# Kernel tuning notes

Measured on AMD Instinct MI355X. Metric: run time of the kernel, lower is better.

Reference implementation:

```python
import jax, jax.numpy as jnp
import numpy as np

N_HEAD = 16  # matches init_kwargs


def _rope_cos_sin(T, head_dim):
    # inv_freq over even indices, as in AdvancedRotaryEmbedding
    inv_freq = 1.0 / (10000.0 ** (jnp.arange(0, head_dim, 2, dtype=jnp.float32) / head_dim))
    t = jnp.arange(T, dtype=jnp.float32)
    freqs = t[:, None] * inv_freq[None, :]  # [T, head_dim/2]
    return jnp.cos(freqs), jnp.sin(freqs)


def _apply_rope(x, cos, sin):
    # x: [B, H, T, D]; cos/sin: [T, D/2] (broadcast over B, H)
    x1, x2 = x[..., 0::2], x[..., 1::2]
    # half-concat layout, faithful to the module's apply_rotary_emb
    return jnp.concatenate([x1 * cos - x2 * sin, x1 * sin + x2 * cos], axis=-1)


def reference(x, Wq, Wk, Wv, Wo):
    B, T, C = x.shape
    H = N_HEAD
    D = C // H
    # QKV projections (torch Linear: y = x @ W.T), then split heads -> [B, H, T, D]
    q = (x @ Wq.T).reshape(B, T, H, D).transpose(0, 2, 1, 3)
    k = (x @ Wk.T).reshape(B, T, H, D).transpose(0, 2, 1, 3)
    v = (x @ Wv.T).reshape(B, T, H, D).transpose(0, 2, 1, 3)
    cos, sin = _rope_cos_sin(T, D)
    cos = cos.astype(x.dtype)
    sin = sin.astype(x.dtype)
    q = _apply_rope(q, cos, sin)
    k = _apply_rope(k, cos, sin)
    # causal SDPA (eval mode -> dropout_p = 0); jax.nn expects [B, T, H, D]
    y = jax.nn.dot_product_attention(
        q.transpose(0, 2, 1, 3),
        k.transpose(0, 2, 1, 3),
        v.transpose(0, 2, 1, 3),
        is_causal=True,
    )  # [B, T, H, D]
    y = y.reshape(B, T, C)
    return y @ Wo.T


def setup_inputs() -> dict:
    key = jax.random.key(0)
    ks = jax.random.split(key, 5)
    B, T, C = 2, 2048, 1024
    s = 1.0 / np.sqrt(C)
    return {
        "x": jax.random.normal(ks[0], (B, T, C), dtype=jnp.float32),
        "Wq": jax.random.normal(ks[1], (C, C), dtype=jnp.float32) * s,
        "Wk": jax.random.normal(ks[2], (C, C), dtype=jnp.float32) * s,
        "Wv": jax.random.normal(ks[3], (C, C), dtype=jnp.float32) * s,
        "Wo": jax.random.normal(ks[4], (C, C), dtype=jnp.float32) * s,
    }
```

## Files before the change

kernel.cpp:

```cpp
#include <hip/hip_runtime.h>
#include <cstdint>
#include <cstddef>

typedef short s16x8 __attribute__((ext_vector_type(8)));
typedef float f32x4 __attribute__((ext_vector_type(4)));

#define MFMA16(a, b, c) __builtin_amdgcn_mfma_f32_16x16x32_bf16((a), (b), (c), 0, 0, 0)

constexpr int LDP = 72;

__device__ __forceinline__ short f2bf(float f) {
    unsigned u = __builtin_bit_cast(unsigned, f);
    u += 0x7FFFu + ((u >> 16) & 1u);
    return (short)(u >> 16);
}
__device__ __forceinline__ float bf2f(short s) {
    unsigned u = ((unsigned)(unsigned short)s) << 16;
    return __builtin_bit_cast(float, u);
}
__device__ __forceinline__ unsigned pack2(float a, float b) {
    return (unsigned)(unsigned short)f2bf(a) | ((unsigned)(unsigned short)f2bf(b) << 16);
}
__device__ __forceinline__ unsigned pack2t(float a, float b) {
    unsigned ua = __builtin_bit_cast(unsigned, a);
    unsigned ub = __builtin_bit_cast(unsigned, b);
    return (ua >> 16) | (ub & 0xFFFF0000u);
}

__device__ __forceinline__ void async_ld16(const void* g, void* l) {
    __builtin_amdgcn_global_load_lds(
        (const __attribute__((address_space(1))) unsigned int*)g,
        (__attribute__((address_space(3))) unsigned int*)l, 16, 0, 0);
}

__global__ __launch_bounds__(256) void convert_kernel(
    const float* __restrict__ x, const float* __restrict__ Wq,
    const float* __restrict__ Wk, const float* __restrict__ Wv,
    const float* __restrict__ Wo, short* __restrict__ xb, short* __restrict__ wb) {
    const size_t f = ((size_t)blockIdx.x * 256 + threadIdx.x) * 8;
    const float* src;
    short* dst;
    if (f < 4194304) { src = x + f; dst = xb + f; }
    else {
        size_t wo = f - 4194304;
        int seg = (int)(wo >> 20);
        const float* ws4[4] = {Wq, Wk, Wv, Wo};
        src = ws4[seg] + (wo & 1048575u);
        dst = wb + wo;
    }
    float4 a = ((const float4*)src)[0];
    float4 b = ((const float4*)src)[1];
    *(uint4*)dst = make_uint4(pack2(a.x, a.y), pack2(a.z, a.w),
                              pack2(b.x, b.y), pack2(b.z, b.w));
}

__global__ __launch_bounds__(256) void qkv_kernel(
    const short* __restrict__ xb, const short* __restrict__ wb,
    short* __restrict__ Qo, short* __restrict__ Ko, short* __restrict__ VTo) {
    __shared__ __align__(16) short sA[128 * 64];
    __shared__ __align__(16) short sB[128 * 64];
    const int tid = threadIdx.x;
    const int w = tid >> 6, lane = tid & 63, quad = lane >> 4, l15 = lane & 15;
    const int wm = w & 1, wn = w >> 1;
    const int bx = blockIdx.x, by = blockIdx.y;
    const int m0 = by * 128;
    const int nb = bx * 128;

    f32x4 acc[4][4];
#pragma unroll
    for (int i = 0; i < 4; i++)
#pragma unroll
        for (int j = 0; j < 4; j++) acc[i][j] = f32x4{0.f, 0.f, 0.f, 0.f};

    for (int kb = 0; kb < 16; kb++) {
        const int k0 = kb * 64;
        if (kb) __syncthreads();
#pragma unroll
        for (int i = 0; i < 4; i++) {
            int c = i * 256 + tid;
            int row = c >> 3, col8 = (c & 7) * 8;
            async_ld16(xb + (size_t)(m0 + row) * 1024 + k0 + col8,
                       &sA[(i * 256 + w * 64) * 8]);
            async_ld16(wb + (size_t)(nb + row) * 1024 + k0 + col8,
                       &sB[(i * 256 + w * 64) * 8]);
        }
        __syncthreads();
#pragma unroll
        for (int ks = 0; ks < 2; ks++) {
            s16x8 av[4], bv[4];
#pragma unroll
            for (int at = 0; at < 4; at++)
                av[at] = *(const s16x8*)&sA[(wm * 64 + at * 16 + l15) * 64 + ks * 32 + quad * 8];
#pragma unroll
            for (int bt = 0; bt < 4; bt++)
                bv[bt] = *(const s16x8*)&sB[(wn * 64 + bt * 16 + l15) * 64 + ks * 32 + quad * 8];
#pragma unroll
            for (int at = 0; at < 4; at++)
#pragma unroll
                for (int bt = 0; bt < 4; bt++)
                    acc[at][bt] = MFMA16(av[at], bv[bt], acc[at][bt]);
        }
    }

    const int wsel = bx >> 3;
    const int h = (bx & 7) * 2 + wn;
    if (wsel == 2) {
#pragma unroll
        for (int at = 0; at < 4; at++) {
            int m = m0 + wm * 64 + at * 16 + quad * 4;
            int b = m >> 11, t0 = m & 2047;
            size_t base = ((size_t)((b * 16 + h) * 64)) * 2048;
#pragma unroll
            for (int bt = 0; bt < 4; bt++) {
                int d = bt * 16 + l15;
                unsigned lo = pack2(acc[at][bt][0], acc[at][bt][1]);
                unsigned hi = pack2(acc[at][bt][2], acc[at][bt][3]);
                *(uint2*)&VTo[base + (size_t)d * 2048 + t0] = make_uint2(lo, hi);
            }
        }
    } else {
        short* Out = (wsel == 0) ? Qo : Ko;
#pragma unroll
        for (int at = 0; at < 4; at++)
#pragma unroll
            for (int r = 0; r < 4; r++) {
                int m = m0 + wm * 64 + at * 16 + quad * 4 + r;
                int b = m >> 11, t = m & 2047;
                size_t base = (((size_t)(b * 16 + h)) * 2048 + t) * 64;
#pragma unroll
                for (int bt = 0; bt < 4; bt++)
                    Out[base + bt * 16 + l15] = f2bf(acc[at][bt][r]);
            }
    }
}

__global__ __launch_bounds__(256) void rope_kernel(short* __restrict__ Q, short* __restrict__ K) {
    const int rid = blockIdx.x * 256 + threadIdx.x;
    const bool isK = (rid & 65536) != 0;
    short* buf = isK ? K : Q;
    const float sc = isK ? 1.0f : 0.18033688011112042f;
    const int r2 = rid & 65535;
    const int t = r2 & 2047;
    short* row = buf + (size_t)r2 * 64;

    unsigned wv[32];
    const uint4* rp = (const uint4*)row;
#pragma unroll
    for (int c = 0; c < 8; c++) {
        uint4 v = rp[c];
        wv[c * 4 + 0] = v.x; wv[c * 4 + 1] = v.y; wv[c * 4 + 2] = v.z; wv[c * 4 + 3] = v.w;
    }
    float y1[32], y2[32];
    const float tf = (float)t;
#pragma unroll
    for (int i = 0; i < 32; i++) {
        float x1 = bf2f((short)(wv[i] & 0xFFFFu));
        float x2 = bf2f((short)(wv[i] >> 16));
        float inv = exp2f((float)i * -0.4152410118609203f);
        float rev = tf * inv * 0.15915494309189535f;
        rev = rev - floorf(rev);
        float sn = __builtin_amdgcn_sinf(rev);
        float cs = __builtin_amdgcn_cosf(rev);
        y1[i] = (x1 * cs - x2 * sn) * sc;
        y2[i] = (x1 * sn + x2 * cs) * sc;
    }
    unsigned ow[32];
#pragma unroll
    for (int i = 0; i < 16; i++) ow[i] = pack2(y1[2 * i], y1[2 * i + 1]);
#pragma unroll
    for (int i = 0; i < 16; i++) ow[16 + i] = pack2(y2[2 * i], y2[2 * i + 1]);
    uint4* wp = (uint4*)row;
#pragma unroll
    for (int c = 0; c < 8; c++)
        wp[c] = make_uint4(ow[c * 4 + 0], ow[c * 4 + 1], ow[c * 4 + 2], ow[c * 4 + 3]);
}

__global__ __launch_bounds__(256) void attn_kernel(
    const short* __restrict__ Q, const short* __restrict__ K,
    const short* __restrict__ VT, short* __restrict__ paO, float* __restrict__ ml) {
    __shared__ __align__(16) short sQP[64 * LDP];
    __shared__ __align__(16) short sK[64 * LDP];
    __shared__ __align__(16) short sVT[64 * LDP];

    const int tid = threadIdx.x;
    const int w = tid >> 6, lane = tid & 63, quad = lane >> 4, l15 = lane & 15;
    const int u = 79 - blockIdx.x;
    const int bh = blockIdx.y;

    int qt, c;
    if (u < 8)       { qt = u; c = 0; }
    else if (u < 24) { int v = u - 8;  qt = 8 + (v >> 1); c = v & 1; }
    else if (u < 48) { int v = u - 24; qt = 16 + v / 3;   c = v - 3 * (qt - 16); }
    else             { int v = u - 48; qt = 24 + (v >> 2); c = v & 3; }
    const int kt0 = c * 8;
    const int kt1 = min(kt0 + 7, qt);

    const short* Qp = Q + (size_t)bh * 2048 * 64;
    const short* Kp = K + (size_t)bh * 2048 * 64;
    const short* Vp = VT + (size_t)bh * 64 * 2048;

    const int ro = tid >> 3, co = (tid & 7) * 8;

    uint4 rK0 = *(const uint4*)(Kp + (size_t)(kt0 * 64 + ro) * 64 + co);
    uint4 rK1 = *(const uint4*)(Kp + (size_t)(kt0 * 64 + ro + 32) * 64 + co);
    uint4 rV0 = *(const uint4*)(Vp + (size_t)ro * 2048 + kt0 * 64 + co);
    uint4 rV1 = *(const uint4*)(Vp + (size_t)(ro + 32) * 2048 + kt0 * 64 + co);

#pragma unroll
    for (int i = 0; i < 2; i++) {
        int p = tid + i * 256;
        int row = p >> 3, c8 = p & 7;
        uint4 v = *(const uint4*)(Qp + (size_t)(qt * 64 + row) * 64 + c8 * 8);
        *(uint4*)&sQP[row * LDP + c8 * 8] = v;
    }
    __syncthreads();
    s16x8 aq[2];
#pragma unroll
    for (int ks = 0; ks < 2; ks++)
        aq[ks] = *(const s16x8*)&sQP[(w * 16 + l15) * LDP + ks * 32 + quad * 8];

    f32x4 o[4];
#pragma unroll
    for (int i = 0; i < 4; i++) o[i] = f32x4{0.f, 0.f, 0.f, 0.f};
    float mrun = -INFINITY;
    float lrun = 0.f;
    const int q_idx = qt * 64 + w * 16 + l15;

    for (int kt = kt0; kt <= kt1; kt++) {
        __syncthreads();
        *(uint4*)&sK[ro * LDP + co] = rK0;
        *(uint4*)&sK[(ro + 32) * LDP + co] = rK1;
        *(uint4*)&sVT[ro * LDP + co] = rV0;
        *(uint4*)&sVT[(ro + 32) * LDP + co] = rV1;
        const int ktn = (kt < kt1) ? kt + 1 : kt;
        rK0 = *(const uint4*)(Kp + (size_t)(ktn * 64 + ro) * 64 + co);
        rK1 = *(const uint4*)(Kp + (size_t)(ktn * 64 + ro + 32) * 64 + co);
        rV0 = *(const uint4*)(Vp + (size_t)ro * 2048 + ktn * 64 + co);
        rV1 = *(const uint4*)(Vp + (size_t)(ro + 32) * 2048 + ktn * 64 + co);
        __syncthreads();

        f32x4 sa[4];
#pragma unroll
        for (int i = 0; i < 4; i++) sa[i] = f32x4{0.f, 0.f, 0.f, 0.f};
#pragma unroll
        for (int ks = 0; ks < 2; ks++) {
#pragma unroll
            for (int ct = 0; ct < 4; ct++) {
                s16x8 kf = *(const s16x8*)&sK[(ct * 16 + l15) * LDP + ks * 32 + quad * 8];
                sa[ct] = MFMA16(kf, aq[ks], sa[ct]);
            }
        }

        float ps[4][4];
#pragma unroll
        for (int ct = 0; ct < 4; ct++)
#pragma unroll
            for (int r = 0; r < 4; r++) ps[ct][r] = sa[ct][r];

        if (kt == qt) {
#pragma unroll
            for (int ct = 0; ct < 4; ct++) {
                int kbase = kt * 64 + ct * 16 + quad * 4;
#pragma unroll
                for (int r = 0; r < 4; r++)
                    if ((kbase + r) > q_idx) ps[ct][r] = -INFINITY;
            }
        }

        float cm[4];
#pragma unroll
        for (int ct = 0; ct < 4; ct++)
            cm[ct] = fmaxf(fmaxf(ps[ct][0], ps[ct][1]), fmaxf(ps[ct][2], ps[ct][3]));
        float mx = fmaxf(fmaxf(cm[0], cm[1]), fmaxf(cm[2], cm[3]));
        mx = fmaxf(mx, __shfl_xor(mx, 16));
        mx = fmaxf(mx, __shfl_xor(mx, 32));
        float mnew = fmaxf(mrun, mx);
        float alpha = exp2f(mrun - mnew);
        mrun = mnew;
        float cs[4];
#pragma unroll
        for (int ct = 0; ct < 4; ct++) {
#pragma unroll
            for (int r = 0; r < 4; r++) ps[ct][r] = exp2f(ps[ct][r] - mnew);
            cs[ct] = (ps[ct][0] + ps[ct][1]) + (ps[ct][2] + ps[ct][3]);
        }
        float psum = (cs[0] + cs[1]) + (cs[2] + cs[3]);
        psum += __shfl_xor(psum, 16);
        psum += __shfl_xor(psum, 32);
        lrun = lrun * alpha + psum;

        float arow[4];
#pragma unroll
        for (int r = 0; r < 4; r++) arow[r] = __shfl(alpha, quad * 4 + r);
#pragma unroll
        for (int ct = 0; ct < 4; ct++)
#pragma unroll
            for (int r = 0; r < 4; r++) o[ct][r] *= arow[r];

#pragma unroll
        for (int ct = 0; ct < 4; ct++) {
            unsigned lo = pack2t(ps[ct][0], ps[ct][1]);
            unsigned hi = pack2t(ps[ct][2], ps[ct][3]);
            *(uint2*)&sQP[(w * 16 + l15) * LDP + ct * 16 + quad * 4] = make_uint2(lo, hi);
        }

#pragma unroll
        for (int ks2 = 0; ks2 < 2; ks2++) {
            s16x8 pa = *(const s16x8*)&sQP[(w * 16 + l15) * LDP + ks2 * 32 + quad * 8];
#pragma unroll
            for (int ct = 0; ct < 4; ct++) {
                s16x8 vb = *(const s16x8*)&sVT[(ct * 16 + l15) * LDP + ks2 * 32 + quad * 8];
                o[ct] = MFMA16(pa, vb, o[ct]);
            }
        }
    }

    const size_t pbase = ((size_t)(bh * 80 + u)) * 4096;
#pragma unroll
    for (int r = 0; r < 4; r++) {
        int row = w * 16 + quad * 4 + r;
#pragma unroll
        for (int ct = 0; ct < 4; ct++)
            paO[pbase + row * 64 + ct * 16 + l15] = f2bf(o[ct][r]);
    }
    if (quad == 0) {
        int mlbase = (bh * 80 + u) * 128;
        ml[mlbase + w * 16 + l15] = mrun;
        ml[mlbase + 64 + w * 16 + l15] = lrun;
    }
}

__global__ __launch_bounds__(256) void combine_kernel(
    const short* __restrict__ paO, const float* __restrict__ ml, short* __restrict__ Y) {
    const int qt = blockIdx.x, bh = blockIdx.y;
    const int b = bh >> 4, h = bh & 15;
    const int nch = (qt >> 3) + 1;
    int base;
    if (qt < 8) base = qt;
    else if (qt < 16) base = 8 + 2 * (qt - 8);
    else if (qt < 24) base = 24 + 3 * (qt - 16);
    else base = 48 + 4 * (qt - 24);

    const int row = threadIdx.x >> 2;
    const int cq = (threadIdx.x & 3) * 16;

    float mi[4], li[4];
    float M = -INFINITY;
    for (int i = 0; i < nch; i++) {
        int mlbase = (bh * 80 + base + i) * 128;
        mi[i] = ml[mlbase + row];
        li[i] = ml[mlbase + 64 + row];
        M = fmaxf(M, mi[i]);
    }
    float L = 0.f, ai[4];
    for (int i = 0; i < nch; i++) {
        ai[i] = exp2f(mi[i] - M);
        L += li[i] * ai[i];
    }
    const float inv = 1.0f / L;

    float acc[16];
#pragma unroll
    for (int j = 0; j < 16; j++) acc[j] = 0.f;
    for (int i = 0; i < nch; i++) {
        const short* p = paO + ((size_t)(bh * 80 + base + i)) * 4096 + row * 64 + cq;
        uint4 v0 = ((const uint4*)p)[0];
        uint4 v1 = ((const uint4*)p)[1];
        unsigned vs[8] = {v0.x, v0.y, v0.z, v0.w, v1.x, v1.y, v1.z, v1.w};
#pragma unroll
        for (int j = 0; j < 8; j++) {
            acc[2 * j + 0] += bf2f((short)(vs[j] & 0xFFFFu)) * ai[i];
            acc[2 * j + 1] += bf2f((short)(vs[j] >> 16)) * ai[i];
        }
    }
    const int t = qt * 64 + row;
    short* yp = Y + ((size_t)(b * 2048 + t)) * 1024 + h * 64 + cq;
    unsigned ow[8];
#pragma unroll
    for (int j = 0; j < 8; j++) ow[j] = pack2(acc[2 * j] * inv, acc[2 * j + 1] * inv);
    ((uint4*)yp)[0] = make_uint4(ow[0], ow[1], ow[2], ow[3]);
    ((uint4*)yp)[1] = make_uint4(ow[4], ow[5], ow[6], ow[7]);
}

__global__ __launch_bounds__(256) void oproj_kernel(
    const short* __restrict__ Yb, const short* __restrict__ Wob, float* __restrict__ out) {
    __shared__ __align__(16) short sA[64 * 64];
    __shared__ __align__(16) short sB[128 * 64];
    const int tid = threadIdx.x;
    const int w = tid >> 6, lane = tid & 63, quad = lane >> 4, l15 = lane & 15;
    const int m0 = blockIdx.y * 64;
    const int nb = blockIdx.x * 128;

    f32x4 acc[4][2];
#pragma unroll
    for (int i = 0; i < 4; i++)
#pragma unroll
        for (int j = 0; j < 2; j++) acc[i][j] = f32x4{0.f, 0.f, 0.f, 0.f};

    for (int kb = 0; kb < 16; kb++) {
        const int k0 = kb * 64;
        if (kb) __syncthreads();
#pragma unroll
        for (int i = 0; i < 2; i++) {
            int c = i * 256 + tid;
            int row = c >> 3, col8 = (c & 7) * 8;
            async_ld16(Yb + (size_t)(m0 + row) * 1024 + k0 + col8,
                       &sA[(i * 256 + w * 64) * 8]);
        }
#pragma unroll
        for (int i = 0; i < 4; i++) {
            int c = i * 256 + tid;
            int row = c >> 3, col8 = (c & 7) * 8;
            async_ld16(Wob + (size_t)(nb + row) * 1024 + k0 + col8,
                       &sB[(i * 256 + w * 64) * 8]);
        }
        __syncthreads();
#pragma unroll
        for (int ks = 0; ks < 2; ks++) {
            s16x8 av[4], bv[2];
#pragma unroll
            for (int at = 0; at < 4; at++)
                av[at] = *(const s16x8*)&sA[(at * 16 + l15) * 64 + ks * 32 + quad * 8];
#pragma unroll
            for (int bt = 0; bt < 2; bt++)
                bv[bt] = *(const s16x8*)&sB[(w * 32 + bt * 16 + l15) * 64 + ks * 32 + quad * 8];
#pragma unroll
            for (int at = 0; at < 4; at++)
#pragma unroll
                for (int bt = 0; bt < 2; bt++)
                    acc[at][bt] = MFMA16(av[at], bv[bt], acc[at][bt]);
        }
    }
#pragma unroll
    for (int at = 0; at < 4; at++)
#pragma unroll
        for (int r = 0; r < 4; r++) {
            int m = m0 + at * 16 + quad * 4 + r;
#pragma unroll
            for (int bt = 0; bt < 2; bt++) {
                int n = nb + w * 32 + bt * 16 + l15;
                out[(size_t)m * 1024 + n] = acc[at][bt][r];
            }
        }
}

extern "C" void kernel_launch(void* const* d_in, const int* in_sizes, int n_in,
                              void* d_out, int out_size, void* d_ws, size_t ws_size,
                              hipStream_t stream) {
    (void)in_sizes; (void)n_in; (void)out_size; (void)ws_size;
    const float* x  = (const float*)d_in[0];
    const float* Wq = (const float*)d_in[1];
    const float* Wk = (const float*)d_in[2];
    const float* Wv = (const float*)d_in[3];
    const float* Wo = (const float*)d_in[4];
    float* out = (float*)d_out;

    const size_t NE = (size_t)2 * 16 * 2048 * 64;
    short* Q   = (short*)d_ws;
    short* K   = Q + NE;
    short* VT  = K + NE;
    short* Y   = VT + NE;
    short* xb  = Y;
    short* wb  = Y + NE;
    short* paO = wb + NE;
    float* ml  = (float*)(paO + (size_t)32 * 80 * 4096);

    convert_kernel<<<4096, 256, 0, stream>>>(x, Wq, Wk, Wv, Wo, xb, wb);
    qkv_kernel<<<dim3(24, 32), 256, 0, stream>>>(xb, wb, Q, K, VT);
    rope_kernel<<<512, 256, 0, stream>>>(Q, K);
    attn_kernel<<<dim3(80, 32), 256, 0, stream>>>(Q, K, VT, paO, ml);
    combine_kernel<<<dim3(32, 32), 256, 0, stream>>>(paO, ml, Y);
    oproj_kernel<<<dim3(8, 64), 256, 0, stream>>>(Y, wb + 3 * 1048576, out);
}
```

Before: 211.7 us.

## Process two query tiles per attention block to reuse K/V loads

Each attention block now handles 128 query rows (two 64-row groups) against each K/V tile, halving K/V global/LDS traffic per query and doubling MFMA work per barrier. The split-K chunk schedule is recomputed for 128-row query tiles, which halves the grid to 1280 blocks, and the combine kernel is reshaped to match. The register prefetch of the next K/V tile is removed, so loads are now synchronous inside the loop. Register pressure rises and there are fewer blocks in flight. The causal mask also covers more wasted work on the diagonal, since both query groups run every key tile up to 2*qt2+1.

Measured after the change: 234.5 us. 10.8% more time.

```diff
diff --git a/kernel.cpp b/kernel.cpp
--- a/kernel.cpp
+++ b/kernel.cpp
@@ -178,178 +178,200 @@
 __global__ __launch_bounds__(256) void attn_kernel(
     const short* __restrict__ Q, const short* __restrict__ K,
     const short* __restrict__ VT, short* __restrict__ paO, float* __restrict__ ml) {
-    __shared__ __align__(16) short sQP[64 * LDP];
+    __shared__ __align__(16) short sQP[128 * LDP];
     __shared__ __align__(16) short sK[64 * LDP];
     __shared__ __align__(16) short sVT[64 * LDP];
 
     const int tid = threadIdx.x;
     const int w = tid >> 6, lane = tid & 63, quad = lane >> 4, l15 = lane & 15;
-    const int u = 79 - blockIdx.x;
+    const int u = 39 - blockIdx.x;
     const int bh = blockIdx.y;
 
-    int qt, c;
-    if (u < 8)       { qt = u; c = 0; }
-    else if (u < 24) { int v = u - 8;  qt = 8 + (v >> 1); c = v & 1; }
-    else if (u < 48) { int v = u - 24; qt = 16 + v / 3;   c = v - 3 * (qt - 16); }
-    else             { int v = u - 48; qt = 24 + (v >> 2); c = v & 3; }
+    int qt2, c;
+    if (u < 4)       { qt2 = u; c = 0; }
+    else if (u < 12) { int v = u - 4;  qt2 = 4 + (v >> 1); c = v & 1; }
+    else if (u < 24) { int v = u - 12; qt2 = 8 + v / 3;    c = v - 3 * (qt2 - 8); }
+    else             { int v = u - 24; qt2 = 12 + (v >> 2); c = v & 3; }
+    const int ktEnd = 2 * qt2 + 1;
     const int kt0 = c * 8;
-    const int kt1 = min(kt0 + 7, qt);
+    const int kt1 = min(kt0 + 7, ktEnd);
 
     const short* Qp = Q + (size_t)bh * 2048 * 64;
     const short* Kp = K + (size_t)bh * 2048 * 64;
     const short* Vp = VT + (size_t)bh * 64 * 2048;
 
-    const int ro = tid >> 3, co = (tid & 7) * 8;
-
-    uint4 rK0 = *(const uint4*)(Kp + (size_t)(kt0 * 64 + ro) * 64 + co);
-    uint4 rK1 = *(const uint4*)(Kp + (size_t)(kt0 * 64 + ro + 32) * 64 + co);
-    uint4 rV0 = *(const uint4*)(Vp + (size_t)ro * 2048 + kt0 * 64 + co);
-    uint4 rV1 = *(const uint4*)(Vp + (size_t)(ro + 32) * 2048 + kt0 * 64 + co);
-
-#pragma unroll
-    for (int i = 0; i < 2; i++) {
+#pragma unroll
+    for (int i = 0; i < 4; i++) {
         int p = tid + i * 256;
         int row = p >> 3, c8 = p & 7;
-        uint4 v = *(const uint4*)(Qp + (size_t)(qt * 64 + row) * 64 + c8 * 8);
+        uint4 v = *(const uint4*)(Qp + (size_t)(qt2 * 128 + row) * 64 + c8 * 8);
         *(uint4*)&sQP[row * LDP + c8 * 8] = v;
     }
     __syncthreads();
-    s16x8 aq[2];
-#pragma unroll
-    for (int ks = 0; ks < 2; ks++)
-        aq[ks] = *(const s16x8*)&sQP[(w * 16 + l15) * LDP + ks * 32 + quad * 8];
-
-    f32x4 o[4];
-#pragma unroll
-    for (int i = 0; i < 4; i++) o[i] = f32x4{0.f, 0.f, 0.f, 0.f};
-    float mrun = -INFINITY;
-    float lrun = 0.f;
-    const int q_idx = qt * 64 + w * 16 + l15;
+    s16x8 aq[2][2];
+#pragma unroll
+    for (int g = 0; g < 2; g++)
+#pragma unroll
+        for (int ks = 0; ks < 2; ks++)
+            aq[g][ks] = *(const s16x8*)&sQP[(g * 64 + w * 16 + l15) * LDP + ks * 32 + quad * 8];
+
+    f32x4 o[2][4];
+#pragma unroll
+    for (int g = 0; g < 2; g++)
+#pragma unroll
+        for (int i = 0; i < 4; i++) o[g][i] = f32x4{0.f, 0.f, 0.f, 0.f};
+    float mrun[2] = {-INFINITY, -INFINITY};
+    float lrun[2] = {0.f, 0.f};
+    const int qidx0 = qt2 * 128 + w * 16 + l15;
+    const int qidx1 = qidx0 + 64;
 
     for (int kt = kt0; kt <= kt1; kt++) {
         __syncthreads();
-        *(uint4*)&sK[ro * LDP + co] = rK0;
-        *(uint4*)&sK[(ro + 32) * LDP + co] = rK1;
-        *(uint4*)&sVT[ro * LDP + co] = rV0;
-        *(uint4*)&sVT[(ro + 32) * LDP + co] = rV1;
-        const int ktn = (kt < kt1) ? kt + 1 : kt;
-        rK0 = *(const uint4*)(Kp + (size_t)(ktn * 64 + ro) * 64 + co);
-        rK1 = *(const uint4*)(Kp + (size_t)(ktn * 64 + ro + 32) * 64 + co);
-        rV0 = *(const uint4*)(Vp + (size_t)ro * 2048 + ktn * 64 + co);
-        rV1 = *(const uint4*)(Vp + (size_t)(ro + 32) * 2048 + ktn * 64 + co);
+#pragma unroll
+        for (int i = 0; i < 2; i++) {
+            int p = tid + i * 256;
+            int row = p >> 3, c8 = p & 7;
+            uint4 kv = *(const uint4*)(Kp + (size_t)(kt * 64 + row) * 64 + c8 * 8);
+            *(uint4*)&sK[row * LDP + c8 * 8] = kv;
+            uint4 vv = *(const uint4*)(Vp + (size_t)row * 2048 + kt * 64 + c8 * 8);
+            *(uint4*)&sVT[row * LDP + c8 * 8] = vv;
+        }
         __syncthreads();
 
-        f32x4 sa[4];
-#pragma unroll
-        for (int i = 0; i < 4; i++) sa[i] = f32x4{0.f, 0.f, 0.f, 0.f};
+        f32x4 sa[2][4];
+#pragma unroll
+        for (int g = 0; g < 2; g++)
+#pragma unroll
+            for (int i = 0; i < 4; i++) sa[g][i] = f32x4{0.f, 0.f, 0.f, 0.f};
 #pragma unroll
         for (int ks = 0; ks < 2; ks++) {
 #pragma unroll
             for (int ct = 0; ct < 4; ct++) {
                 s16x8 kf = *(const s16x8*)&sK[(ct * 16 + l15) * LDP + ks * 32 + quad * 8];
-                sa[ct] = MFMA16(kf, aq[ks], sa[ct]);
-            }
-        }
-
-        float ps[4][4];
-#pragma unroll
-        for (int ct = 0; ct < 4; ct++)
-#pragma unroll
-            for (int r = 0; r < 4; r++) ps[ct][r] = sa[ct][r];
-
-        if (kt == qt) {
+                sa[0][ct] = MFMA16(kf, aq[0][ks], sa[0][ct]);
+                sa[1][ct] = MFMA16(kf, aq[1][ks], sa[1][ct]);
+            }
+        }
+
+        float ps[2][4][4];
+#pragma unroll
+        for (int g = 0; g < 2; g++)
+#pragma unroll
+            for (int ct = 0; ct < 4; ct++)
+#pragma unroll
+                for (int r = 0; r < 4; r++) ps[g][ct][r] = sa[g][ct][r];
+
+        if (kt >= 2 * qt2) {
 #pragma unroll
             for (int ct = 0; ct < 4; ct++) {
                 int kbase = kt * 64 + ct * 16 + quad * 4;
 #pragma unroll
-                for (int r = 0; r < 4; r++)
-                    if ((kbase + r) > q_idx) ps[ct][r] = -INFINITY;
-            }
-        }
-
-        float cm[4];
-#pragma unroll
-        for (int ct = 0; ct < 4; ct++)
-            cm[ct] = fmaxf(fmaxf(ps[ct][0], ps[ct][1]), fmaxf(ps[ct][2], ps[ct][3]));
-        float mx = fmaxf(fmaxf(cm[0], cm[1]), fmaxf(cm[2], cm[3]));
-        mx = fmaxf(mx, __shfl_xor(mx, 16));
-        mx = fmaxf(mx, __shfl_xor(mx, 32));
-        float mnew = fmaxf(mrun, mx);
-        float alpha = exp2f(mrun - mnew);
-        mrun = mnew;
-        float cs[4];
-#pragma unroll
-        for (int ct = 0; ct < 4; ct++) {
-#pragma unroll
-            for (int r = 0; r < 4; r++) ps[ct][r] = exp2f(ps[ct][r] - mnew);
-            cs[ct] = (ps[ct][0] + ps[ct][1]) + (ps[ct][2] + ps[ct][3]);
-        }
-        float psum = (cs[0] + cs[1]) + (cs[2] + cs[3]);
-        psum += __shfl_xor(psum, 16);
-        psum += __shfl_xor(psum, 32);
-        lrun = lrun * alpha + psum;
-
-        float arow[4];
-#pragma unroll
-        for (int r = 0; r < 4; r++) arow[r] = __shfl(alpha, quad * 4 + r);
-#pragma unroll
-        for (int ct = 0; ct < 4; ct++)
-#pragma unroll
-            for (int r = 0; r < 4; r++) o[ct][r] *= arow[r];
-
-#pragma unroll
-        for (int ct = 0; ct < 4; ct++) {
-            unsigned lo = pack2t(ps[ct][0], ps[ct][1]);
-            unsigned hi = pack2t(ps[ct][2], ps[ct][3]);
-            *(uint2*)&sQP[(w * 16 + l15) * LDP + ct * 16 + quad * 4] = make_uint2(lo, hi);
-        }
+                for (int r = 0; r < 4; r++) {
+                    if ((kbase + r) > qidx0) ps[0][ct][r] = -INFINITY;
+                    if ((kbase + r) > qidx1) ps[1][ct][r] = -INFINITY;
+                }
+            }
+        }
+
+        float alpha[2];
+#pragma unroll
+        for (int g = 0; g < 2; g++) {
+            float cm[4];
+#pragma unroll
+            for (int ct = 0; ct < 4; ct++)
+                cm[ct] = fmaxf(fmaxf(ps[g][ct][0], ps[g][ct][1]), fmaxf(ps[g][ct][2], ps[g][ct][3]));
+            float mx = fmaxf(fmaxf(cm[0], cm[1]), fmaxf(cm[2], cm[3]));
+            mx = fmaxf(mx, __shfl_xor(mx, 16));
+            mx = fmaxf(mx, __shfl_xor(mx, 32));
+            float mnew = fmaxf(mrun[g], mx);
+            alpha[g] = exp2f(mrun[g] - mnew);
+            mrun[g] = mnew;
+            float cs[4];
+#pragma unroll
+            for (int ct = 0; ct < 4; ct++) {
+#pragma unroll
+                for (int r = 0; r < 4; r++) ps[g][ct][r] = exp2f(ps[g][ct][r] - mnew);
+                cs[ct] = (ps[g][ct][0] + ps[g][ct][1]) + (ps[g][ct][2] + ps[g][ct][3]);
+            }
+            float psum = (cs[0] + cs[1]) + (cs[2] + cs[3]);
+            psum += __shfl_xor(psum, 16);
+            psum += __shfl_xor(psum, 32);
+            lrun[g] = lrun[g] * alpha[g] + psum;
+        }
+
+#pragma unroll
+        for (int g = 0; g < 2; g++) {
+            float arow[4];
+#pragma unroll
+            for (int r = 0; r < 4; r++) arow[r] = __shfl(alpha[g], quad * 4 + r);
+#pragma unroll
+            for (int ct = 0; ct < 4; ct++)
+#pragma unroll
+                for (int r = 0; r < 4; r++) o[g][ct][r] *= arow[r];
+        }
+
+#pragma unroll
+        for (int g = 0; g < 2; g++)
+#pragma unroll
+            for (int ct = 0; ct < 4; ct++) {
+                unsigned lo = pack2t(ps[g][ct][0], ps[g][ct][1]);
+                unsigned hi = pack2t(ps[g][ct][2], ps[g][ct][3]);
+                *(uint2*)&sQP[(g * 64 + w * 16 + l15) * LDP + ct * 16 + quad * 4] = make_uint2(lo, hi);
+            }
 
 #pragma unroll
         for (int ks2 = 0; ks2 < 2; ks2++) {
-            s16x8 pa = *(const s16x8*)&sQP[(w * 16 + l15) * LDP + ks2 * 32 + quad * 8];
+            s16x8 pa0 = *(const s16x8*)&sQP[(w * 16 + l15) * LDP + ks2 * 32 + quad * 8];
+            s16x8 pa1 = *(const s16x8*)&sQP[(64 + w * 16 + l15) * LDP + ks2 * 32 + quad * 8];
 #pragma unroll
             for (int ct = 0; ct < 4; ct++) {
                 s16x8 vb = *(const s16x8*)&sVT[(ct * 16 + l15) * LDP + ks2 * 32 + quad * 8];
-                o[ct] = MFMA16(pa, vb, o[ct]);
-            }
-        }
-    }
-
-    const size_t pbase = ((size_t)(bh * 80 + u)) * 4096;
-#pragma unroll
-    for (int r = 0; r < 4; r++) {
-        int row = w * 16 + quad * 4 + r;
-#pragma unroll
-        for (int ct = 0; ct < 4; ct++)
-            paO[pbase + row * 64 + ct * 16 + l15] = f2bf(o[ct][r]);
-    }
+                o[0][ct] = MFMA16(pa0, vb, o[0][ct]);
+                o[1][ct] = MFMA16(pa1, vb, o[1][ct]);
+            }
+        }
+    }
+
+    const size_t pbase = ((size_t)(bh * 40 + u)) * 8192;
+#pragma unroll
+    for (int g = 0; g < 2; g++)
+#pragma unroll
+        for (int r = 0; r < 4; r++) {
+            int row = g * 64 + w * 16 + quad * 4 + r;
+#pragma unroll
+            for (int ct = 0; ct < 4; ct++)
+                paO[pbase + row * 64 + ct * 16 + l15] = f2bf(o[g][ct][r]);
+        }
     if (quad == 0) {
-        int mlbase = (bh * 80 + u) * 128;
-        ml[mlbase + w * 16 + l15] = mrun;
-        ml[mlbase + 64 + w * 16 + l15] = lrun;
+        int mlbase = (bh * 40 + u) * 256;
+#pragma unroll
+        for (int g = 0; g < 2; g++) {
+            ml[mlbase + g * 64 + w * 16 + l15] = mrun[g];
+            ml[mlbase + 128 + g * 64 + w * 16 + l15] = lrun[g];
+        }
     }
 }
 
 __global__ __launch_bounds__(256) void combine_kernel(
     const short* __restrict__ paO, const float* __restrict__ ml, short* __restrict__ Y) {
-    const int qt = blockIdx.x, bh = blockIdx.y;
+    const int qt2 = blockIdx.x, bh = blockIdx.y;
     const int b = bh >> 4, h = bh & 15;
-    const int nch = (qt >> 3) + 1;
+    const int nch = (qt2 >> 2) + 1;
     int base;
-    if (qt < 8) base = qt;
-    else if (qt < 16) base = 8 + 2 * (qt - 8);
-    else if (qt < 24) base = 24 + 3 * (qt - 16);
-    else base = 48 + 4 * (qt - 24);
-
-    const int row = threadIdx.x >> 2;
-    const int cq = (threadIdx.x & 3) * 16;
+    if (qt2 < 4) base = qt2;
+    else if (qt2 < 8) base = 4 + 2 * (qt2 - 4);
+    else if (qt2 < 12) base = 12 + 3 * (qt2 - 8);
+    else base = 24 + 4 * (qt2 - 12);
+
+    const int row = threadIdx.x >> 1;
+    const int cq = (threadIdx.x & 1) * 32;
 
     float mi[4], li[4];
     float M = -INFINITY;
     for (int i = 0; i < nch; i++) {
-        int mlbase = (bh * 80 + base + i) * 128;
+        int mlbase = (bh * 40 + base + i) * 256;
         mi[i] = ml[mlbase + row];
-        li[i] = ml[mlbase + 64 + row];
+        li[i] = ml[mlbase + 128 + row];
         M = fmaxf(M, mi[i]);
     }
     float L = 0.f, ai[4];
@@ -359,27 +381,32 @@
     }
     const float inv = 1.0f / L;
 
-    float acc[16];
-#pragma unroll
-    for (int j = 0; j < 16; j++) acc[j] = 0.f;
+    float acc[32];
+#pragma unroll
+    for (int j = 0; j < 32; j++) acc[j] = 0.f;
     for (int i = 0; i < nch; i++) {
-        const short* p = paO + ((size_t)(bh * 80 + base + i)) * 4096 + row * 64 + cq;
-        uint4 v0 = ((const uint4*)p)[0];
-        uint4 v1 = ((const uint4*)p)[1];
-        unsigned vs[8] = {v0.x, v0.y, v0.z, v0.w, v1.x, v1.y, v1.z, v1.w};
-#pragma unroll
-        for (int j = 0; j < 8; j++) {
-            acc[2 * j + 0] += bf2f((short)(vs[j] & 0xFFFFu)) * ai[i];
-            acc[2 * j + 1] += bf2f((short)(vs[j] >> 16)) * ai[i];
-        }
-    }
-    const int t = qt * 64 + row;
+        const short* p = paO + ((size_t)(bh * 40 + base + i)) * 8192 + row * 64 + cq;
+#pragma unroll
+        for (int q = 0; q < 4; q++) {
+            uint4 v = ((const uint4*)p)[q];
+            unsigned vs[4] = {v.x, v.y, v.z, v.w};
+#pragma unroll
+            for (int j = 0; j < 4; j++) {
+                acc[q * 8 + 2 * j + 0] += bf2f((short)(vs[j] & 0xFFFFu)) * ai[i];
+                acc[q * 8 + 2 * j + 1] += bf2f((short)(vs[j] >> 16)) * ai[i];
+            }
+        }
+    }
+    const int t = qt2 * 128 + row;
     short* yp = Y + ((size_t)(b * 2048 + t)) * 1024 + h * 64 + cq;
-    unsigned ow[8];
-#pragma unroll
-    for (int j = 0; j < 8; j++) ow[j] = pack2(acc[2 * j] * inv, acc[2 * j + 1] * inv);
-    ((uint4*)yp)[0] = make_uint4(ow[0], ow[1], ow[2], ow[3]);
-    ((uint4*)yp)[1] = make_uint4(ow[4], ow[5], ow[6], ow[7]);
+#pragma unroll
+    for (int q = 0; q < 4; q++) {
+        unsigned ow[4];
+#pragma unroll
+        for (int j = 0; j < 4; j++)
+            ow[j] = pack2(acc[q * 8 + 2 * j] * inv, acc[q * 8 + 2 * j + 1] * inv);
+        ((uint4*)yp)[q] = make_uint4(ow[0], ow[1], ow[2], ow[3]);
+    }
 }
 
 __global__ __launch_bounds__(256) void oproj_kernel(
@@ -463,12 +490,12 @@
     short* xb  = Y;
     short* wb  = Y + NE;
     short* paO = wb + NE;
-    float* ml  = (float*)(paO + (size_t)32 * 80 * 4096);
+    float* ml  = (float*)(paO + (size_t)32 * 40 * 8192);
 
     convert_kernel<<<4096, 256, 0, stream>>>(x, Wq, Wk, Wv, Wo, xb, wb);
     qkv_kernel<<<dim3(24, 32), 256, 0, stream>>>(xb, wb, Q, K, VT);
     rope_kernel<<<512, 256, 0, stream>>>(Q, K);
-    attn_kernel<<<dim3(80, 32), 256, 0, stream>>>(Q, K, VT, paO, ml);
-    combine_kernel<<<dim3(32, 32), 256, 0, stream>>>(paO, ml, Y);
+    attn_kernel<<<dim3(40, 32), 256, 0, stream>>>(Q, K, VT, paO, ml);
+    combine_kernel<<<dim3(16, 32), 256, 0, stream>>>(paO, ml, Y);
     oproj_kernel<<<dim3(8, 64), 256, 0, stream>>>(Y, wb + 3 * 1048576, out);
 }
```

## Widen attention KV tile to 128 keys and drop register prefetch

Applied to the files above, without the earlier changes.

Each attention loop iteration now processes 128 keys instead of 64, with a wider LDS stride for the P and V^T buffers. The register-staged prefetch of the next K/V tile is replaced by direct global-to-LDS loads inside the loop. This halves the loop iterations and barrier/softmax-reduction overhead per key. In exchange it loses load/compute overlap, raises LDS use and register pressure, and computes masked keys beyond the diagonal.

Result: no change. 212.4 us (+0.3%).

```diff
diff --git a/kernel.cpp b/kernel.cpp
--- a/kernel.cpp
+++ b/kernel.cpp
@@ -8,6 +8,7 @@
 #define MFMA16(a, b, c) __builtin_amdgcn_mfma_f32_16x16x32_bf16((a), (b), (c), 0, 0, 0)
 
 constexpr int LDP = 72;
+constexpr int LDW = 136;
 
 __device__ __forceinline__ short f2bf(float f) {
     unsigned u = __builtin_bit_cast(unsigned, f);
@@ -178,9 +179,9 @@
 __global__ __launch_bounds__(256) void attn_kernel(
     const short* __restrict__ Q, const short* __restrict__ K,
     const short* __restrict__ VT, short* __restrict__ paO, float* __restrict__ ml) {
-    __shared__ __align__(16) short sQP[64 * LDP];
-    __shared__ __align__(16) short sK[64 * LDP];
-    __shared__ __align__(16) short sVT[64 * LDP];
+    __shared__ __align__(16) short sQP[64 * LDW];
+    __shared__ __align__(16) short sK[128 * LDP];
+    __shared__ __align__(16) short sVT[64 * LDW];
 
     const int tid = threadIdx.x;
     const int w = tid >> 6, lane = tid & 63, quad = lane >> 4, l15 = lane & 15;
@@ -192,32 +193,26 @@
     else if (u < 24) { int v = u - 8;  qt = 8 + (v >> 1); c = v & 1; }
     else if (u < 48) { int v = u - 24; qt = 16 + v / 3;   c = v - 3 * (qt - 16); }
     else             { int v = u - 48; qt = 24 + (v >> 2); c = v & 3; }
-    const int kt0 = c * 8;
-    const int kt1 = min(kt0 + 7, qt);
+    const int kbDiag = qt >> 1;
+    const int kb0 = c * 4;
+    const int kb1 = min(kb0 + 3, kbDiag);
 
     const short* Qp = Q + (size_t)bh * 2048 * 64;
     const short* Kp = K + (size_t)bh * 2048 * 64;
     const short* Vp = VT + (size_t)bh * 64 * 2048;
-
-    const int ro = tid >> 3, co = (tid & 7) * 8;
-
-    uint4 rK0 = *(const uint4*)(Kp + (size_t)(kt0 * 64 + ro) * 64 + co);
-    uint4 rK1 = *(const uint4*)(Kp + (size_t)(kt0 * 64 + ro + 32) * 64 + co);
-    uint4 rV0 = *(const uint4*)(Vp + (size_t)ro * 2048 + kt0 * 64 + co);
-    uint4 rV1 = *(const uint4*)(Vp + (size_t)(ro + 32) * 2048 + kt0 * 64 + co);
 
 #pragma unroll
     for (int i = 0; i < 2; i++) {
         int p = tid + i * 256;
         int row = p >> 3, c8 = p & 7;
         uint4 v = *(const uint4*)(Qp + (size_t)(qt * 64 + row) * 64 + c8 * 8);
-        *(uint4*)&sQP[row * LDP + c8 * 8] = v;
+        *(uint4*)&sQP[row * LDW + c8 * 8] = v;
     }
     __syncthreads();
     s16x8 aq[2];
 #pragma unroll
     for (int ks = 0; ks < 2; ks++)
-        aq[ks] = *(const s16x8*)&sQP[(w * 16 + l15) * LDP + ks * 32 + quad * 8];
+        aq[ks] = *(const s16x8*)&sQP[(w * 16 + l15) * LDW + ks * 32 + quad * 8];
 
     f32x4 o[4];
 #pragma unroll
@@ -226,65 +221,70 @@
     float lrun = 0.f;
     const int q_idx = qt * 64 + w * 16 + l15;
 
-    for (int kt = kt0; kt <= kt1; kt++) {
+    for (int kb = kb0; kb <= kb1; kb++) {
         __syncthreads();
-        *(uint4*)&sK[ro * LDP + co] = rK0;
-        *(uint4*)&sK[(ro + 32) * LDP + co] = rK1;
-        *(uint4*)&sVT[ro * LDP + co] = rV0;
-        *(uint4*)&sVT[(ro + 32) * LDP + co] = rV1;
-        const int ktn = (kt < kt1) ? kt + 1 : kt;
-        rK0 = *(const uint4*)(Kp + (size_t)(ktn * 64 + ro) * 64 + co);
-        rK1 = *(const uint4*)(Kp + (size_t)(ktn * 64 + ro + 32) * 64 + co);
-        rV0 = *(const uint4*)(Vp + (size_t)ro * 2048 + ktn * 64 + co);
-        rV1 = *(const uint4*)(Vp + (size_t)(ro + 32) * 2048 + ktn * 64 + co);
+#pragma unroll
+        for (int i = 0; i < 4; i++) {
+            int p = tid + i * 256;
+            {
+                int row = p >> 3, c8 = p & 7;
+                uint4 kv = *(const uint4*)(Kp + (size_t)(kb * 128 + row) * 64 + c8 * 8);
+                *(uint4*)&sK[row * LDP + c8 * 8] = kv;
+            }
+            {
+                int row = p >> 4, c16 = p & 15;
+                uint4 vv = *(const uint4*)(Vp + (size_t)row * 2048 + kb * 128 + c16 * 8);
+                *(uint4*)&sVT[row * LDW + c16 * 8] = vv;
+            }
+        }
         __syncthreads();
 
-        f32x4 sa[4];
-#pragma unroll
-        for (int i = 0; i < 4; i++) sa[i] = f32x4{0.f, 0.f, 0.f, 0.f};
+        f32x4 sa[8];
+#pragma unroll
+        for (int i = 0; i < 8; i++) sa[i] = f32x4{0.f, 0.f, 0.f, 0.f};
 #pragma unroll
         for (int ks = 0; ks < 2; ks++) {
 #pragma unroll
-            for (int ct = 0; ct < 4; ct++) {
+            for (int ct = 0; ct < 8; ct++) {
                 s16x8 kf = *(const s16x8*)&sK[(ct * 16 + l15) * LDP + ks * 32 + quad * 8];
                 sa[ct] = MFMA16(kf, aq[ks], sa[ct]);
             }
         }
 
-        float ps[4][4];
-#pragma unroll
-        for (int ct = 0; ct < 4; ct++)
+        float ps[8][4];
+#pragma unroll
+        for (int ct = 0; ct < 8; ct++)
 #pragma unroll
             for (int r = 0; r < 4; r++) ps[ct][r] = sa[ct][r];
 
-        if (kt == qt) {
-#pragma unroll
-            for (int ct = 0; ct < 4; ct++) {
-                int kbase = kt * 64 + ct * 16 + quad * 4;
+        if (kb == kbDiag) {
+#pragma unroll
+            for (int ct = 0; ct < 8; ct++) {
+                int kbase = kb * 128 + ct * 16 + quad * 4;
 #pragma unroll
                 for (int r = 0; r < 4; r++)
                     if ((kbase + r) > q_idx) ps[ct][r] = -INFINITY;
             }
         }
 
-        float cm[4];
-#pragma unroll
-        for (int ct = 0; ct < 4; ct++)
+        float cm[8];
+#pragma unroll
+        for (int ct = 0; ct < 8; ct++)
             cm[ct] = fmaxf(fmaxf(ps[ct][0], ps[ct][1]), fmaxf(ps[ct][2], ps[ct][3]));
-        float mx = fmaxf(fmaxf(cm[0], cm[1]), fmaxf(cm[2], cm[3]));
+        float mx = fmaxf(fmaxf(fmaxf(cm[0], cm[1]), fmaxf(cm[2], cm[3])),
+                         fmaxf(fmaxf(cm[4], cm[5]), fmaxf(cm[6], cm[7])));
         mx = fmaxf(mx, __shfl_xor(mx, 16));
         mx = fmaxf(mx, __shfl_xor(mx, 32));
         float mnew = fmaxf(mrun, mx);
         float alpha = exp2f(mrun - mnew);
         mrun = mnew;
-        float cs[4];
-#pragma unroll
-        for (int ct = 0; ct < 4; ct++) {
+#pragma unroll
+        for (int ct = 0; ct < 8; ct++) {
 #pragma unroll
             for (int r = 0; r < 4; r++) ps[ct][r] = exp2f(ps[ct][r] - mnew);
-            cs[ct] = (ps[ct][0] + ps[ct][1]) + (ps[ct][2] + ps[ct][3]);
-        }
-        float psum = (cs[0] + cs[1]) + (cs[2] + cs[3]);
+            cm[ct] = (ps[ct][0] + ps[ct][1]) + (ps[ct][2] + ps[ct][3]);
+        }
+        float psum = ((cm[0] + cm[1]) + (cm[2] + cm[3])) + ((cm[4] + cm[5]) + (cm[6] + cm[7]));
         psum += __shfl_xor(psum, 16);
         psum += __shfl_xor(psum, 32);
         lrun = lrun * alpha + psum;
@@ -298,18 +298,18 @@
             for (int r = 0; r < 4; r++) o[ct][r] *= arow[r];
 
 #pragma unroll
-        for (int ct = 0; ct < 4; ct++) {
+        for (int ct = 0; ct < 8; ct++) {
             unsigned lo = pack2t(ps[ct][0], ps[ct][1]);
             unsigned hi = pack2t(ps[ct][2], ps[ct][3]);
-            *(uint2*)&sQP[(w * 16 + l15) * LDP + ct * 16 + quad * 4] = make_uint2(lo, hi);
-        }
-
-#pragma unroll
-        for (int ks2 = 0; ks2 < 2; ks2++) {
-            s16x8 pa = *(const s16x8*)&sQP[(w * 16 + l15) * LDP + ks2 * 32 + quad * 8];
+            *(uint2*)&sQP[(w * 16 + l15) * LDW + ct * 16 + quad * 4] = make_uint2(lo, hi);
+        }
+
+#pragma unroll
+        for (int ks2 = 0; ks2 < 4; ks2++) {
+            s16x8 pa = *(const s16x8*)&sQP[(w * 16 + l15) * LDW + ks2 * 32 + quad * 8];
 #pragma unroll
             for (int ct = 0; ct < 4; ct++) {
-                s16x8 vb = *(const s16x8*)&sVT[(ct * 16 + l15) * LDP + ks2 * 32 + quad * 8];
+                s16x8 vb = *(const s16x8*)&sVT[(ct * 16 + l15) * LDW + ks2 * 32 + quad * 8];
                 o[ct] = MFMA16(pa, vb, o[ct]);
             }
         }
```
